# Kernel optimization log

Hardware: AMD Instinct MI355X
Metric: run time of the kernel (lower is better)

Reference implementation:

```python
import jax, jax.numpy as jnp
import numpy as np

B, N, D = 8, 2048, 256

def setup_inputs() -> dict:
    key = jax.random.key(0)
    ks = jax.random.split(key, 8)
    sc = 1.0 / np.sqrt(D)
    return {
        "x": jax.random.normal(ks[0], (B, N, D), dtype=jnp.float32),
        "W_fp": jax.random.normal(ks[1], (D, D), dtype=jnp.float32) * sc,
        "b_fp": jnp.zeros((D,), dtype=jnp.float32),
        "w_s": jax.random.normal(ks[2], (D,), dtype=jnp.float32) * sc,
        "b_s": jnp.zeros((), dtype=jnp.float32),
        "W_rp": jax.random.normal(ks[3], (D, D), dtype=jnp.float32) * sc,
        "b_rp": jnp.zeros((D,), dtype=jnp.float32),
        "W_gp": jax.random.normal(ks[4], (D, D), dtype=jnp.float32) * sc,
        "b_gp": jnp.zeros((D,), dtype=jnp.float32),
        "gamma": jnp.ones((D,), dtype=jnp.float32),
        "beta": jnp.zeros((D,), dtype=jnp.float32),
    }

def reference(x, W_fp, b_fp, w_s, b_s, W_rp, b_rp, W_gp, b_gp, gamma, beta):
    # feature projection: [B, N, D]
    proj = jnp.einsum('bnd,de->bne', x, W_fp) + b_fp
    # F.normalize(p=2, dim=-1) with eps=1e-12
    nrm = jnp.sqrt(jnp.sum(proj * proj, axis=-1, keepdims=True))
    xn = proj / jnp.maximum(nrm, 1e-12)
    # cosine similarity matrix [B, N, N]
    sim = jnp.einsum('bnd,bmd->bnm', xn, xn)
    # adj_scaler: Linear(D,1)+sigmoid is constant along the broadcast axis ->
    # compute per-node scalar once [B, N] (same math as the O(N^2*D) expand)
    s = jax.nn.sigmoid(jnp.einsum('bnd,d->bn', proj, w_s) + b_s)
    scaler = jnp.clip(0.5 * (s[:, :, None] + s[:, None, :]), 1e-6, 1.0)
    adj = jnp.maximum(scaler * sim, 1e-6)  # clamp(min=1e-6)
    degree = jnp.maximum(jnp.sum(adj, axis=2, keepdims=True), 1e-6)
    norm_adj = adj / degree
    # aggregation + region projection
    region = jnp.einsum('bnm,bmd->bnd', norm_adj, proj)
    region = jnp.einsum('bnd,de->bne', region, W_rp) + b_rp
    # global pooling + projection: [B, 1, D]
    g = jnp.mean(region, axis=1, keepdims=True)
    g = jnp.einsum('bnd,de->bne', g, W_gp) + b_gp
    input_global = jnp.mean(x, axis=1, keepdims=True)
    h = g + input_global
    # LayerNorm (eps=1e-5)
    mu = jnp.mean(h, axis=-1, keepdims=True)
    var = jnp.mean((h - mu) ** 2, axis=-1, keepdims=True)
    out = (h - mu) / jnp.sqrt(var + 1e-5) * gamma + beta
    return out, adj
```

## Files before the change

kernel.cpp:

```cpp
#include <hip/hip_runtime.h>
#include <hip/hip_bf16.h>
#include <math.h>

#define Bn 8
#define Nn 2048
#define Dn 256

typedef short short8 __attribute__((ext_vector_type(8)));
typedef float floatx4 __attribute__((ext_vector_type(4)));

__device__ __forceinline__ short f2bf_bits(float f) {
    __bf16 h = (__bf16)f;
    return __builtin_bit_cast(short, h);
}

__device__ __forceinline__ float bf2f(short s) {
    unsigned u = ((unsigned)(unsigned short)s) << 16;
    return __builtin_bit_cast(float, u);
}

__device__ __forceinline__ void gl_lds16(const void* gsrc, void* ldst) {
    __builtin_amdgcn_global_load_lds(
        (const __attribute__((address_space(1))) void*)gsrc,
        (__attribute__((address_space(3))) void*)ldst, 16, 0, 0);
}

__device__ __forceinline__ float sigmoidf_(float z) {
    return 1.0f / (1.0f + __expf(-z));
}


__global__ __launch_bounds__(256) void k_transpose(const float* __restrict__ W,
                                                   short* __restrict__ Wt) {
    __shared__ float Ts[64][65];
    const int t = threadIdx.x;
    const int dt0 = blockIdx.x * 64, et0 = blockIdx.y * 64;
    const int ro = t >> 4, co = (t & 15) * 4;
    #pragma unroll
    for (int rr = 0; rr < 4; ++rr) {
        int row = rr * 16 + ro;
        float4 v = *(const float4*)(W + (size_t)(dt0 + row) * Dn + et0 + co);
        Ts[row][co + 0] = v.x; Ts[row][co + 1] = v.y;
        Ts[row][co + 2] = v.z; Ts[row][co + 3] = v.w;
    }
    __syncthreads();
    const int e = t >> 2, cd0 = (t & 3) * 16;
    short8 a, b;
    #pragma unroll
    for (int i = 0; i < 8; ++i) {
        a[i] = f2bf_bits(Ts[cd0 + i][e]);
        b[i] = f2bf_bits(Ts[cd0 + 8 + i][e]);
    }
    *(short8*)(Wt + (size_t)(et0 + e) * Dn + dt0 + cd0) = a;
    *(short8*)(Wt + (size_t)(et0 + e) * Dn + dt0 + cd0 + 8) = b;
}


__global__ __launch_bounds__(512) void k_projxn(
    const float* __restrict__ x, const short* __restrict__ Wt,
    const float* __restrict__ b_fp, const float* __restrict__ w_s,
    short* __restrict__ xn, float* __restrict__ sdot, float* __restrict__ nrm,
    float* __restrict__ xpart) {
    __shared__ __align__(16) short As[64 * 64];
    __shared__ __align__(16) short Bs[256 * 64];
    __shared__ float xsumS[8 * 256];
    __shared__ float redW[2][64];
    __shared__ float redN[2][64];
    const int t = threadIdx.x;
    const int bm = blockIdx.x * 64;
    const int lane = t & 63, wv = t >> 6;
    const int wm = (wv & 3) * 16;
    const int jh = wv >> 2;
    const int l15 = lane & 15, q = lane >> 4;

    for (int i = t; i < 2048; i += 512) xsumS[i] = 0.f;

    floatx4 acc[8];
    #pragma unroll
    for (int j = 0; j < 8; ++j) acc[j] = (floatx4){0.f, 0.f, 0.f, 0.f};

    const int rA = t >> 3, cA = (t & 7) * 8;
    const int rB = t >> 3, cB = (t & 7) * 8;

    for (int k0 = 0; k0 < Dn; k0 += 64) {
        const float* gp = x + (size_t)(bm + rA) * Dn + k0 + cA;
        float4 v0 = *(const float4*)gp;
        float4 v1 = *(const float4*)(gp + 4);
        short8 o0;
        o0[0] = f2bf_bits(v0.x); o0[1] = f2bf_bits(v0.y);
        o0[2] = f2bf_bits(v0.z); o0[3] = f2bf_bits(v0.w);
        o0[4] = f2bf_bits(v1.x); o0[5] = f2bf_bits(v1.y);
        o0[6] = f2bf_bits(v1.z); o0[7] = f2bf_bits(v1.w);
        *(short8*)(As + rA * 64 + cA) = o0;
        #pragma unroll
        for (int cc = 0; cc < 4; ++cc)
            gl_lds16(Wt + (size_t)(cc * 64 + rB) * Dn + k0 + cB,
                     Bs + (cc * 64 + rB) * 64 + cB);
        __syncthreads();
        #pragma unroll
        for (int ks = 0; ks < 2; ++ks) {
            short8 af = *(const short8*)(As + (wm + l15) * 64 + ks * 32 + q * 8);
            #pragma unroll
            for (int jj = 0; jj < 8; ++jj) {
                short8 bfr = *(const short8*)(Bs + (jh * 128 + jj * 16 + l15) * 64 + ks * 32 + q * 8);
                acc[jj] = __builtin_amdgcn_mfma_f32_16x16x32_bf16(af, bfr, acc[jj], 0, 0, 0);
            }
        }
        {
            float s = 0.f;
            #pragma unroll
            for (int r = 0; r < 8; ++r)
                s += bf2f(As[(wv * 8 + r) * 64 + lane]);
            xsumS[wv * 256 + k0 + lane] += s;
        }
        __syncthreads();
    }
    if (t < 256) {
        float xs = 0.f;
        #pragma unroll
        for (int w = 0; w < 8; ++w) xs += xsumS[w * 256 + t];
        xpart[(size_t)blockIdx.x * Dn + t] = xs;
    }
    float bfv[8], wsv[8];
    #pragma unroll
    for (int jj = 0; jj < 8; ++jj) {
        bfv[jj] = b_fp[jh * 128 + jj * 16 + l15];
        wsv[jj] = w_s[jh * 128 + jj * 16 + l15];
    }
    float vv[4][8];
    #pragma unroll
    for (int reg = 0; reg < 4; ++reg) {
        float pw = 0.f, pn = 0.f;
        #pragma unroll
        for (int jj = 0; jj < 8; ++jj) {
            float v = acc[jj][reg] + bfv[jj];
            vv[reg][jj] = v;
            pw += v * wsv[jj];
            pn += v * v;
        }
        #pragma unroll
        for (int m = 1; m < 16; m <<= 1) {
            pw += __shfl_xor(pw, m);
            pn += __shfl_xor(pn, m);
        }
        if (l15 == 0) {
            redW[jh][wm + q * 4 + reg] = pw;
            redN[jh][wm + q * 4 + reg] = pn;
        }
    }
    __syncthreads();
    #pragma unroll
    for (int reg = 0; reg < 4; ++reg) {
        int lr = wm + q * 4 + reg;
        float pw = redW[0][lr] + redW[1][lr];
        float pn = redN[0][lr] + redN[1][lr];
        float nc = fmaxf(sqrtf(pn), 1e-12f);
        float inv = 1.0f / nc;
        int row = bm + lr;
        size_t rbase = (size_t)row * Dn + jh * 128 + l15;
        #pragma unroll
        for (int jj = 0; jj < 8; ++jj)
            xn[rbase + jj * 16] = f2bf_bits(vv[reg][jj] * inv);
        if (jh == 0 && l15 == 0) {
            sdot[row] = pw;
            nrm[row] = nc;
        }
    }
}


__global__ __launch_bounds__(512) void k_sim(
    const short* __restrict__ xn, const float* __restrict__ sdot,
    const float* __restrict__ b_s, float* __restrict__ adj,
    float* __restrict__ deg_part) {
    __shared__ __align__(16) short As[128 * 64];
    __shared__ __align__(16) short Bs[256 * 64];
    __shared__ float degS[4][128];
    const int t = threadIdx.x;
    int lin = (blockIdx.z * 16 + blockIdx.y) * 8 + blockIdx.x;
    const int b = lin & 7;
    const int pos = lin >> 3;
    const int by = pos >> 3, cx = pos & 7;
    const int bm = by * 128;
    const int bn = cx * 256;
    const int lane = t & 63, wv = t >> 6;
    const int wm = (wv >> 2) * 64;
    const int wn = (wv & 3) * 64;
    const int l15 = lane & 15, q4 = lane >> 4;
    const int rr = t >> 3, c8 = (t & 7) * 8;
    const short* xb = xn + (size_t)b * Nn * Dn;

    floatx4 acc[4][4];
    #pragma unroll
    for (int i = 0; i < 4; ++i)
        #pragma unroll
        for (int j = 0; j < 4; ++j) acc[i][j] = (floatx4){0.f, 0.f, 0.f, 0.f};

    for (int k0 = 0; k0 < Dn; k0 += 64) {
        #pragma unroll
        for (int cc = 0; cc < 2; ++cc) {
            int r = cc * 64 + rr;
            gl_lds16(xb + (size_t)(bm + r) * Dn + k0 + c8, As + r * 64 + c8);
        }
        #pragma unroll
        for (int cc = 0; cc < 4; ++cc) {
            int r = cc * 64 + rr;
            gl_lds16(xb + (size_t)(bn + r) * Dn + k0 + c8, Bs + r * 64 + c8);
        }
        __syncthreads();
        #pragma unroll
        for (int ks = 0; ks < 2; ++ks) {
            short8 af[4], bfr[4];
            #pragma unroll
            for (int i = 0; i < 4; ++i)
                af[i] = *(const short8*)(As + (wm + i * 16 + l15) * 64 + ks * 32 + q4 * 8);
            #pragma unroll
            for (int j = 0; j < 4; ++j)
                bfr[j] = *(const short8*)(Bs + (wn + j * 16 + l15) * 64 + ks * 32 + q4 * 8);
            #pragma unroll
            for (int i = 0; i < 4; ++i)
                #pragma unroll
                for (int j = 0; j < 4; ++j)
                    acc[i][j] = __builtin_amdgcn_mfma_f32_16x16x32_bf16(bfr[j], af[i], acc[i][j], 0, 0, 0);
        }
        __syncthreads();
    }
    const float bsv = b_s[0];
    float srow[4];
    #pragma unroll
    for (int i = 0; i < 4; ++i)
        srow[i] = sigmoidf_(sdot[b * Nn + bm + wm + i * 16 + l15] + bsv);
    float scol[4][4];
    #pragma unroll
    for (int j = 0; j < 4; ++j)
        #pragma unroll
        for (int reg = 0; reg < 4; ++reg)
            scol[j][reg] = sigmoidf_(sdot[b * Nn + bn + wn + j * 16 + q4 * 4 + reg] + bsv);
    #pragma unroll
    for (int i = 0; i < 4; ++i) {
        float rs = 0.f;
        size_t rbase = ((size_t)b * Nn + (bm + wm + i * 16 + l15)) * Nn + bn + wn + q4 * 4;
        #pragma unroll
        for (int j = 0; j < 4; ++j) {
            float4 o;
            float sc;
            sc = fminf(fmaxf(0.5f * (srow[i] + scol[j][0]), 1e-6f), 1.0f);
            o.x = fmaxf(sc * acc[i][j][0], 1e-6f);
            sc = fminf(fmaxf(0.5f * (srow[i] + scol[j][1]), 1e-6f), 1.0f);
            o.y = fmaxf(sc * acc[i][j][1], 1e-6f);
            sc = fminf(fmaxf(0.5f * (srow[i] + scol[j][2]), 1e-6f), 1.0f);
            o.z = fmaxf(sc * acc[i][j][2], 1e-6f);
            sc = fminf(fmaxf(0.5f * (srow[i] + scol[j][3]), 1e-6f), 1.0f);
            o.w = fmaxf(sc * acc[i][j][3], 1e-6f);
            *(float4*)(adj + rbase + (size_t)j * 16) = o;
            rs += o.x + o.y + o.z + o.w;
        }
        rs += __shfl_xor(rs, 16);
        rs += __shfl_xor(rs, 32);
        if (q4 == 0) degS[wv & 3][wm + i * 16 + l15] = rs;
    }
    __syncthreads();
    if (t < 128)
        deg_part[((size_t)(b * 8 + cx)) * Nn + bm + t] =
            degS[0][t] + degS[1][t] + degS[2][t] + degS[3][t];
}


__global__ __launch_bounds__(256) void k_deg(const float* __restrict__ deg_part,
                                             float* __restrict__ invdeg) {
    int b = blockIdx.x, t = blockIdx.y * 256 + threadIdx.x;
    float s = 0.f;
    #pragma unroll
    for (int cx = 0; cx < 8; ++cx)
        s += deg_part[((size_t)(b * 8 + cx)) * Nn + t];
    invdeg[b * Nn + t] = 1.0f / fmaxf(s, 1e-6f);
}


__global__ __launch_bounds__(1024) void k_colsum(
    const float* __restrict__ adj, const float* __restrict__ invdeg,
    const short* __restrict__ xn, const float* __restrict__ nrm,
    float* __restrict__ gpart) {
    int b = blockIdx.x, ck = blockIdx.y, t = threadIdx.x;
    __shared__ float invS[Nn];
    __shared__ float part[64][64];
    __shared__ float csL[64];
    __shared__ float gQ[4][Dn];
    invS[t] = invdeg[b * Nn + t];
    invS[t + 1024] = invdeg[b * Nn + t + 1024];
    __syncthreads();
    const int lc = (t & 15) * 4;
    const int rg = t >> 4;
    const int c0 = ck * 64;
    float sx = 0.f, sy = 0.f, sz = 0.f, sw = 0.f;
    for (int r = rg; r < Nn; r += 64) {
        float4 v = *(const float4*)(adj + ((size_t)b * Nn + r) * Nn + c0 + lc);
        float w = invS[r];
        sx += v.x * w; sy += v.y * w; sz += v.z * w; sw += v.w * w;
    }
    part[rg][lc + 0] = sx; part[rg][lc + 1] = sy;
    part[rg][lc + 2] = sz; part[rg][lc + 3] = sw;
    __syncthreads();
    if (t < 64) {
        float s = 0.f;
        #pragma unroll
        for (int g = 0; g < 64; ++g) s += part[g][t];
        csL[t] = s * nrm[b * Nn + c0 + t];
    }
    __syncthreads();
    {
        int h = t >> 8, d = t & 255;
        float g = 0.f;
        #pragma unroll 4
        for (int mi = 0; mi < 16; ++mi) {
            int m = h * 16 + mi;
            g += csL[m] * bf2f(xn[((size_t)(b * Nn + c0 + m)) * Dn + d]);
        }
        gQ[h][d] = g;
    }
    __syncthreads();
    if (t < Dn)
        gpart[(b * 32 + ck) * Dn + t] = gQ[0][t] + gQ[1][t] + gQ[2][t] + gQ[3][t];
}


__global__ __launch_bounds__(1024) void k_final2(
    const float* __restrict__ gpart, const float* __restrict__ xpart,
    const float* __restrict__ W_rp, const float* __restrict__ b_rp,
    const float* __restrict__ W_gp, const float* __restrict__ b_gp,
    const float* __restrict__ gamma, const float* __restrict__ beta,
    float* __restrict__ out) {
    int b = blockIdx.x, t = threadIdx.x;
    const int d = t & 255, c4 = t >> 8;
    __shared__ float pS[4][Dn];
    __shared__ float xS[4][Dn];
    __shared__ float gp_s[Dn];
    __shared__ float xm_s[Dn];
    __shared__ float g1_s[Dn];
    __shared__ float red[8];
    {
        float gs = 0.f, xs = 0.f;
        #pragma unroll
        for (int k = 0; k < 8; ++k) {
            int ck = c4 * 8 + k;
            gs += gpart[(b * 32 + ck) * Dn + d];
            xs += xpart[(b * 32 + ck) * Dn + d];
        }
        pS[c4][d] = gs;
        xS[c4][d] = xs;
    }
    __syncthreads();
    if (t < Dn) {
        gp_s[t] = (pS[0][t] + pS[1][t] + pS[2][t] + pS[3][t]) * (1.0f / Nn);
        xm_s[t] = (xS[0][t] + xS[1][t] + xS[2][t] + xS[3][t]) * (1.0f / Nn);
    }
    __syncthreads();
    {
        float m1 = 0.f;
        #pragma unroll 4
        for (int i = 0; i < 64; ++i) {
            int dd = c4 * 64 + i;
            m1 += gp_s[dd] * W_rp[dd * Dn + d];
        }
        pS[c4][d] = m1;
    }
    __syncthreads();
    if (t < Dn) g1_s[t] = b_rp[t] + pS[0][t] + pS[1][t] + pS[2][t] + pS[3][t];
    __syncthreads();
    {
        float m2 = 0.f;
        #pragma unroll 4
        for (int i = 0; i < 64; ++i) {
            int ee = c4 * 64 + i;
            m2 += g1_s[ee] * W_gp[ee * Dn + d];
        }
        pS[c4][d] = m2;
    }
    __syncthreads();
    float h = 0.f;
    if (t < Dn) {
        h = b_gp[t] + pS[0][t] + pS[1][t] + pS[2][t] + pS[3][t] + xm_s[t];
        float sum = h;
        #pragma unroll
        for (int m = 1; m < 64; m <<= 1) sum += __shfl_xor(sum, m);
        if ((t & 63) == 0) red[t >> 6] = sum;
    }
    __syncthreads();
    float mu = (red[0] + red[1] + red[2] + red[3]) * (1.0f / Dn);
    if (t < Dn) {
        float dv = h - mu;
        float s2 = dv * dv;
        #pragma unroll
        for (int m = 1; m < 64; m <<= 1) s2 += __shfl_xor(s2, m);
        if ((t & 63) == 0) red[4 + (t >> 6)] = s2;
    }
    __syncthreads();
    if (t < Dn) {
        float dv = h - mu;
        float var = (red[4] + red[5] + red[6] + red[7]) * (1.0f / Dn);
        out[b * Dn + t] = dv * rsqrtf(var + 1e-5f) * gamma[t] + beta[t];
    }
}


extern "C" void kernel_launch(void* const* d_in, const int* in_sizes, int n_in,
                              void* d_out, int out_size, void* d_ws, size_t ws_size,
                              hipStream_t stream) {
    const float* x     = (const float*)d_in[0];
    const float* W_fp  = (const float*)d_in[1];
    const float* b_fp  = (const float*)d_in[2];
    const float* w_s   = (const float*)d_in[3];
    const float* b_s   = (const float*)d_in[4];
    const float* W_rp  = (const float*)d_in[5];
    const float* b_rp  = (const float*)d_in[6];
    const float* W_gp  = (const float*)d_in[7];
    const float* b_gp  = (const float*)d_in[8];
    const float* gamma = (const float*)d_in[9];
    const float* beta  = (const float*)d_in[10];

    float* out = (float*)d_out;
    float* adj = out + Bn * Dn;

    char* ws = (char*)d_ws;
    short* xn     = (short*)(ws);
    short* Wt     = (short*)(ws + 8388608);
    float* sdot   = (float*)(ws + 8519680);
    float* nrm    = (float*)(ws + 8585216);
    float* degp   = (float*)(ws + 8650752);
    float* invdeg = (float*)(ws + 9175040);
    float* gpart  = (float*)(ws + 9699328);
    float* xpart  = (float*)(ws + 9961472);

    k_transpose<<<dim3(4, 4), 256, 0, stream>>>(W_fp, Wt);
    k_projxn<<<(Bn * Nn) / 64, 512, 0, stream>>>(x, Wt, b_fp, w_s, xn, sdot, nrm, xpart);
    k_sim<<<dim3(8, 16, 8), 512, 0, stream>>>(xn, sdot, b_s, adj, degp);
    k_deg<<<dim3(Bn, 8), 256, 0, stream>>>(degp, invdeg);
    k_colsum<<<dim3(Bn, 32), 1024, 0, stream>>>(adj, invdeg, xn, nrm, gpart);
    k_final2<<<Bn, 1024, 0, stream>>>(gpart, xpart, W_rp, b_rp, W_gp, b_gp, gamma, beta, out);
}
```

Before: 237.8 us.

## Fuse all stages into one cooperative persistent kernel with grid syncs

Replaces the six separate kernel launches (transpose, projection, similarity, degree, column-sum, final) with a single cooperative kernel of 256 blocks that runs each stage in turn, separated by grid-wide barriers, and reuses one shared-memory buffer across stages. The goal is to remove launch overhead and inter-kernel gaps. In exchange, parallelism is capped at 256 blocks, so the sim stage loops over tiles and the colsum stage uses 512 threads instead of 1024. The later stages also leave many blocks idle while a few do the work.

```diff
diff --git a/kernel.cpp b/kernel.cpp
--- a/kernel.cpp
+++ b/kernel.cpp
@@ -1,6 +1,9 @@
 #include <hip/hip_runtime.h>
+#include <hip/hip_cooperative_groups.h>
 #include <hip/hip_bf16.h>
 #include <math.h>
+
+namespace cg = cooperative_groups;
 
 #define Bn 8
 #define Nn 2048
@@ -30,375 +33,384 @@
 }
 
 
-__global__ __launch_bounds__(256) void k_transpose(const float* __restrict__ W,
-                                                   short* __restrict__ Wt) {
-    __shared__ float Ts[64][65];
-    const int t = threadIdx.x;
-    const int dt0 = blockIdx.x * 64, et0 = blockIdx.y * 64;
-    const int ro = t >> 4, co = (t & 15) * 4;
-    #pragma unroll
-    for (int rr = 0; rr < 4; ++rr) {
-        int row = rr * 16 + ro;
-        float4 v = *(const float4*)(W + (size_t)(dt0 + row) * Dn + et0 + co);
-        Ts[row][co + 0] = v.x; Ts[row][co + 1] = v.y;
-        Ts[row][co + 2] = v.z; Ts[row][co + 3] = v.w;
-    }
-    __syncthreads();
-    const int e = t >> 2, cd0 = (t & 3) * 16;
-    short8 a, b;
-    #pragma unroll
-    for (int i = 0; i < 8; ++i) {
-        a[i] = f2bf_bits(Ts[cd0 + i][e]);
-        b[i] = f2bf_bits(Ts[cd0 + 8 + i][e]);
-    }
-    *(short8*)(Wt + (size_t)(et0 + e) * Dn + dt0 + cd0) = a;
-    *(short8*)(Wt + (size_t)(et0 + e) * Dn + dt0 + cd0 + 8) = b;
-}
-
-
-__global__ __launch_bounds__(512) void k_projxn(
-    const float* __restrict__ x, const short* __restrict__ Wt,
+__global__ __launch_bounds__(512) void k_fused(
+    const float* __restrict__ x, const float* __restrict__ W_fp,
+    short* __restrict__ Wt,
     const float* __restrict__ b_fp, const float* __restrict__ w_s,
+    const float* __restrict__ b_s,
     short* __restrict__ xn, float* __restrict__ sdot, float* __restrict__ nrm,
-    float* __restrict__ xpart) {
-    __shared__ __align__(16) short As[64 * 64];
-    __shared__ __align__(16) short Bs[256 * 64];
-    __shared__ float xsumS[8 * 256];
-    __shared__ float redW[2][64];
-    __shared__ float redN[2][64];
-    const int t = threadIdx.x;
-    const int bm = blockIdx.x * 64;
-    const int lane = t & 63, wv = t >> 6;
-    const int wm = (wv & 3) * 16;
-    const int jh = wv >> 2;
-    const int l15 = lane & 15, q = lane >> 4;
-
-    for (int i = t; i < 2048; i += 512) xsumS[i] = 0.f;
-
-    floatx4 acc[8];
-    #pragma unroll
-    for (int j = 0; j < 8; ++j) acc[j] = (floatx4){0.f, 0.f, 0.f, 0.f};
-
-    const int rA = t >> 3, cA = (t & 7) * 8;
-    const int rB = t >> 3, cB = (t & 7) * 8;
-
-    for (int k0 = 0; k0 < Dn; k0 += 64) {
-        const float* gp = x + (size_t)(bm + rA) * Dn + k0 + cA;
-        float4 v0 = *(const float4*)gp;
-        float4 v1 = *(const float4*)(gp + 4);
-        short8 o0;
-        o0[0] = f2bf_bits(v0.x); o0[1] = f2bf_bits(v0.y);
-        o0[2] = f2bf_bits(v0.z); o0[3] = f2bf_bits(v0.w);
-        o0[4] = f2bf_bits(v1.x); o0[5] = f2bf_bits(v1.y);
-        o0[6] = f2bf_bits(v1.z); o0[7] = f2bf_bits(v1.w);
-        *(short8*)(As + rA * 64 + cA) = o0;
-        #pragma unroll
-        for (int cc = 0; cc < 4; ++cc)
-            gl_lds16(Wt + (size_t)(cc * 64 + rB) * Dn + k0 + cB,
-                     Bs + (cc * 64 + rB) * 64 + cB);
-        __syncthreads();
-        #pragma unroll
-        for (int ks = 0; ks < 2; ++ks) {
-            short8 af = *(const short8*)(As + (wm + l15) * 64 + ks * 32 + q * 8);
-            #pragma unroll
-            for (int jj = 0; jj < 8; ++jj) {
-                short8 bfr = *(const short8*)(Bs + (jh * 128 + jj * 16 + l15) * 64 + ks * 32 + q * 8);
-                acc[jj] = __builtin_amdgcn_mfma_f32_16x16x32_bf16(af, bfr, acc[jj], 0, 0, 0);
-            }
-        }
-        {
-            float s = 0.f;
-            #pragma unroll
-            for (int r = 0; r < 8; ++r)
-                s += bf2f(As[(wv * 8 + r) * 64 + lane]);
-            xsumS[wv * 256 + k0 + lane] += s;
-        }
-        __syncthreads();
-    }
-    if (t < 256) {
-        float xs = 0.f;
-        #pragma unroll
-        for (int w = 0; w < 8; ++w) xs += xsumS[w * 256 + t];
-        xpart[(size_t)blockIdx.x * Dn + t] = xs;
-    }
-    float bfv[8], wsv[8];
-    #pragma unroll
-    for (int jj = 0; jj < 8; ++jj) {
-        bfv[jj] = b_fp[jh * 128 + jj * 16 + l15];
-        wsv[jj] = w_s[jh * 128 + jj * 16 + l15];
-    }
-    float vv[4][8];
-    #pragma unroll
-    for (int reg = 0; reg < 4; ++reg) {
-        float pw = 0.f, pn = 0.f;
-        #pragma unroll
-        for (int jj = 0; jj < 8; ++jj) {
-            float v = acc[jj][reg] + bfv[jj];
-            vv[reg][jj] = v;
-            pw += v * wsv[jj];
-            pn += v * v;
-        }
-        #pragma unroll
-        for (int m = 1; m < 16; m <<= 1) {
-            pw += __shfl_xor(pw, m);
-            pn += __shfl_xor(pn, m);
-        }
-        if (l15 == 0) {
-            redW[jh][wm + q * 4 + reg] = pw;
-            redN[jh][wm + q * 4 + reg] = pn;
-        }
-    }
-    __syncthreads();
-    #pragma unroll
-    for (int reg = 0; reg < 4; ++reg) {
-        int lr = wm + q * 4 + reg;
-        float pw = redW[0][lr] + redW[1][lr];
-        float pn = redN[0][lr] + redN[1][lr];
-        float nc = fmaxf(sqrtf(pn), 1e-12f);
-        float inv = 1.0f / nc;
-        int row = bm + lr;
-        size_t rbase = (size_t)row * Dn + jh * 128 + l15;
-        #pragma unroll
-        for (int jj = 0; jj < 8; ++jj)
-            xn[rbase + jj * 16] = f2bf_bits(vv[reg][jj] * inv);
-        if (jh == 0 && l15 == 0) {
-            sdot[row] = pw;
-            nrm[row] = nc;
-        }
-    }
-}
-
-
-__global__ __launch_bounds__(512) void k_sim(
-    const short* __restrict__ xn, const float* __restrict__ sdot,
-    const float* __restrict__ b_s, float* __restrict__ adj,
-    float* __restrict__ deg_part) {
-    __shared__ __align__(16) short As[128 * 64];
-    __shared__ __align__(16) short Bs[256 * 64];
-    __shared__ float degS[4][128];
-    const int t = threadIdx.x;
-    int lin = (blockIdx.z * 16 + blockIdx.y) * 8 + blockIdx.x;
-    const int b = lin & 7;
-    const int pos = lin >> 3;
-    const int by = pos >> 3, cx = pos & 7;
-    const int bm = by * 128;
-    const int bn = cx * 256;
-    const int lane = t & 63, wv = t >> 6;
-    const int wm = (wv >> 2) * 64;
-    const int wn = (wv & 3) * 64;
-    const int l15 = lane & 15, q4 = lane >> 4;
-    const int rr = t >> 3, c8 = (t & 7) * 8;
-    const short* xb = xn + (size_t)b * Nn * Dn;
-
-    floatx4 acc[4][4];
-    #pragma unroll
-    for (int i = 0; i < 4; ++i)
-        #pragma unroll
-        for (int j = 0; j < 4; ++j) acc[i][j] = (floatx4){0.f, 0.f, 0.f, 0.f};
-
-    for (int k0 = 0; k0 < Dn; k0 += 64) {
-        #pragma unroll
-        for (int cc = 0; cc < 2; ++cc) {
-            int r = cc * 64 + rr;
-            gl_lds16(xb + (size_t)(bm + r) * Dn + k0 + c8, As + r * 64 + c8);
-        }
-        #pragma unroll
-        for (int cc = 0; cc < 4; ++cc) {
-            int r = cc * 64 + rr;
-            gl_lds16(xb + (size_t)(bn + r) * Dn + k0 + c8, Bs + r * 64 + c8);
-        }
-        __syncthreads();
-        #pragma unroll
-        for (int ks = 0; ks < 2; ++ks) {
-            short8 af[4], bfr[4];
-            #pragma unroll
-            for (int i = 0; i < 4; ++i)
-                af[i] = *(const short8*)(As + (wm + i * 16 + l15) * 64 + ks * 32 + q4 * 8);
-            #pragma unroll
-            for (int j = 0; j < 4; ++j)
-                bfr[j] = *(const short8*)(Bs + (wn + j * 16 + l15) * 64 + ks * 32 + q4 * 8);
-            #pragma unroll
-            for (int i = 0; i < 4; ++i)
-                #pragma unroll
-                for (int j = 0; j < 4; ++j)
-                    acc[i][j] = __builtin_amdgcn_mfma_f32_16x16x32_bf16(bfr[j], af[i], acc[i][j], 0, 0, 0);
-        }
-        __syncthreads();
-    }
-    const float bsv = b_s[0];
-    float srow[4];
-    #pragma unroll
-    for (int i = 0; i < 4; ++i)
-        srow[i] = sigmoidf_(sdot[b * Nn + bm + wm + i * 16 + l15] + bsv);
-    float scol[4][4];
-    #pragma unroll
-    for (int j = 0; j < 4; ++j)
-        #pragma unroll
-        for (int reg = 0; reg < 4; ++reg)
-            scol[j][reg] = sigmoidf_(sdot[b * Nn + bn + wn + j * 16 + q4 * 4 + reg] + bsv);
-    #pragma unroll
-    for (int i = 0; i < 4; ++i) {
-        float rs = 0.f;
-        size_t rbase = ((size_t)b * Nn + (bm + wm + i * 16 + l15)) * Nn + bn + wn + q4 * 4;
-        #pragma unroll
-        for (int j = 0; j < 4; ++j) {
-            float4 o;
-            float sc;
-            sc = fminf(fmaxf(0.5f * (srow[i] + scol[j][0]), 1e-6f), 1.0f);
-            o.x = fmaxf(sc * acc[i][j][0], 1e-6f);
-            sc = fminf(fmaxf(0.5f * (srow[i] + scol[j][1]), 1e-6f), 1.0f);
-            o.y = fmaxf(sc * acc[i][j][1], 1e-6f);
-            sc = fminf(fmaxf(0.5f * (srow[i] + scol[j][2]), 1e-6f), 1.0f);
-            o.z = fmaxf(sc * acc[i][j][2], 1e-6f);
-            sc = fminf(fmaxf(0.5f * (srow[i] + scol[j][3]), 1e-6f), 1.0f);
-            o.w = fmaxf(sc * acc[i][j][3], 1e-6f);
-            *(float4*)(adj + rbase + (size_t)j * 16) = o;
-            rs += o.x + o.y + o.z + o.w;
-        }
-        rs += __shfl_xor(rs, 16);
-        rs += __shfl_xor(rs, 32);
-        if (q4 == 0) degS[wv & 3][wm + i * 16 + l15] = rs;
-    }
-    __syncthreads();
-    if (t < 128)
-        deg_part[((size_t)(b * 8 + cx)) * Nn + bm + t] =
-            degS[0][t] + degS[1][t] + degS[2][t] + degS[3][t];
-}
-
-
-__global__ __launch_bounds__(256) void k_deg(const float* __restrict__ deg_part,
-                                             float* __restrict__ invdeg) {
-    int b = blockIdx.x, t = blockIdx.y * 256 + threadIdx.x;
-    float s = 0.f;
-    #pragma unroll
-    for (int cx = 0; cx < 8; ++cx)
-        s += deg_part[((size_t)(b * 8 + cx)) * Nn + t];
-    invdeg[b * Nn + t] = 1.0f / fmaxf(s, 1e-6f);
-}
-
-
-__global__ __launch_bounds__(1024) void k_colsum(
-    const float* __restrict__ adj, const float* __restrict__ invdeg,
-    const short* __restrict__ xn, const float* __restrict__ nrm,
-    float* __restrict__ gpart) {
-    int b = blockIdx.x, ck = blockIdx.y, t = threadIdx.x;
-    __shared__ float invS[Nn];
-    __shared__ float part[64][64];
-    __shared__ float csL[64];
-    __shared__ float gQ[4][Dn];
-    invS[t] = invdeg[b * Nn + t];
-    invS[t + 1024] = invdeg[b * Nn + t + 1024];
-    __syncthreads();
-    const int lc = (t & 15) * 4;
-    const int rg = t >> 4;
-    const int c0 = ck * 64;
-    float sx = 0.f, sy = 0.f, sz = 0.f, sw = 0.f;
-    for (int r = rg; r < Nn; r += 64) {
-        float4 v = *(const float4*)(adj + ((size_t)b * Nn + r) * Nn + c0 + lc);
-        float w = invS[r];
-        sx += v.x * w; sy += v.y * w; sz += v.z * w; sw += v.w * w;
-    }
-    part[rg][lc + 0] = sx; part[rg][lc + 1] = sy;
-    part[rg][lc + 2] = sz; part[rg][lc + 3] = sw;
-    __syncthreads();
-    if (t < 64) {
-        float s = 0.f;
-        #pragma unroll
-        for (int g = 0; g < 64; ++g) s += part[g][t];
-        csL[t] = s * nrm[b * Nn + c0 + t];
-    }
-    __syncthreads();
-    {
-        int h = t >> 8, d = t & 255;
-        float g = 0.f;
-        #pragma unroll 4
-        for (int mi = 0; mi < 16; ++mi) {
-            int m = h * 16 + mi;
-            g += csL[m] * bf2f(xn[((size_t)(b * Nn + c0 + m)) * Dn + d]);
-        }
-        gQ[h][d] = g;
-    }
-    __syncthreads();
-    if (t < Dn)
-        gpart[(b * 32 + ck) * Dn + t] = gQ[0][t] + gQ[1][t] + gQ[2][t] + gQ[3][t];
-}
-
-
-__global__ __launch_bounds__(1024) void k_final2(
-    const float* __restrict__ gpart, const float* __restrict__ xpart,
+    float* __restrict__ xpart,
+    float* __restrict__ adj, float* __restrict__ degp,
+    float* __restrict__ invdeg, float* __restrict__ gpart,
     const float* __restrict__ W_rp, const float* __restrict__ b_rp,
     const float* __restrict__ W_gp, const float* __restrict__ b_gp,
     const float* __restrict__ gamma, const float* __restrict__ beta,
     float* __restrict__ out) {
-    int b = blockIdx.x, t = threadIdx.x;
-    const int d = t & 255, c4 = t >> 8;
-    __shared__ float pS[4][Dn];
-    __shared__ float xS[4][Dn];
-    __shared__ float gp_s[Dn];
-    __shared__ float xm_s[Dn];
-    __shared__ float g1_s[Dn];
-    __shared__ float red[8];
+    cg::grid_group grid = cg::this_grid();
+    __shared__ __align__(16) char SM[51200];
+    const int t = threadIdx.x;
+    const int bid = blockIdx.x;
+    const int lane = t & 63, wv = t >> 6;
+    const int l15 = lane & 15, q = lane >> 4;
+
+    if (bid < 16) {
+        float (*Ts)[65] = (float(*)[65])SM;
+        const int dt0 = (bid >> 2) * 64, et0 = (bid & 3) * 64;
+        if (t < 256) {
+            const int ro = t >> 4, co = (t & 15) * 4;
+            #pragma unroll
+            for (int rr = 0; rr < 4; ++rr) {
+                int row = rr * 16 + ro;
+                float4 v = *(const float4*)(W_fp + (size_t)(dt0 + row) * Dn + et0 + co);
+                Ts[row][co + 0] = v.x; Ts[row][co + 1] = v.y;
+                Ts[row][co + 2] = v.z; Ts[row][co + 3] = v.w;
+            }
+        }
+        __syncthreads();
+        if (t < 256) {
+            const int e = t >> 2, cd0 = (t & 3) * 16;
+            short8 a, b;
+            #pragma unroll
+            for (int i = 0; i < 8; ++i) {
+                a[i] = f2bf_bits(Ts[cd0 + i][e]);
+                b[i] = f2bf_bits(Ts[cd0 + 8 + i][e]);
+            }
+            *(short8*)(Wt + (size_t)(et0 + e) * Dn + dt0 + cd0) = a;
+            *(short8*)(Wt + (size_t)(et0 + e) * Dn + dt0 + cd0 + 8) = b;
+        }
+    }
+    grid.sync();
+
     {
-        float gs = 0.f, xs = 0.f;
-        #pragma unroll
-        for (int k = 0; k < 8; ++k) {
-            int ck = c4 * 8 + k;
-            gs += gpart[(b * 32 + ck) * Dn + d];
-            xs += xpart[(b * 32 + ck) * Dn + d];
-        }
-        pS[c4][d] = gs;
-        xS[c4][d] = xs;
-    }
-    __syncthreads();
-    if (t < Dn) {
-        gp_s[t] = (pS[0][t] + pS[1][t] + pS[2][t] + pS[3][t]) * (1.0f / Nn);
-        xm_s[t] = (xS[0][t] + xS[1][t] + xS[2][t] + xS[3][t]) * (1.0f / Nn);
-    }
-    __syncthreads();
+        short* As = (short*)SM;
+        short* Bs = (short*)(SM + 8192);
+        float* xsumS = (float*)(SM + 40960);
+        float* redW = (float*)(SM + 49152);
+        float* redN = (float*)(SM + 49664);
+        const int bm = bid * 64;
+        const int wm = (wv & 3) * 16;
+        const int jh = wv >> 2;
+
+        for (int i = t; i < 2048; i += 512) xsumS[i] = 0.f;
+
+        floatx4 acc[8];
+        #pragma unroll
+        for (int j = 0; j < 8; ++j) acc[j] = (floatx4){0.f, 0.f, 0.f, 0.f};
+
+        const int rA = t >> 3, cA = (t & 7) * 8;
+        const int rB = t >> 3, cB = (t & 7) * 8;
+
+        for (int k0 = 0; k0 < Dn; k0 += 64) {
+            const float* gp = x + (size_t)(bm + rA) * Dn + k0 + cA;
+            float4 v0 = *(const float4*)gp;
+            float4 v1 = *(const float4*)(gp + 4);
+            short8 o0;
+            o0[0] = f2bf_bits(v0.x); o0[1] = f2bf_bits(v0.y);
+            o0[2] = f2bf_bits(v0.z); o0[3] = f2bf_bits(v0.w);
+            o0[4] = f2bf_bits(v1.x); o0[5] = f2bf_bits(v1.y);
+            o0[6] = f2bf_bits(v1.z); o0[7] = f2bf_bits(v1.w);
+            *(short8*)(As + rA * 64 + cA) = o0;
+            #pragma unroll
+            for (int cc = 0; cc < 4; ++cc)
+                gl_lds16(Wt + (size_t)(cc * 64 + rB) * Dn + k0 + cB,
+                         Bs + (cc * 64 + rB) * 64 + cB);
+            __syncthreads();
+            #pragma unroll
+            for (int ks = 0; ks < 2; ++ks) {
+                short8 af = *(const short8*)(As + (wm + l15) * 64 + ks * 32 + q * 8);
+                #pragma unroll
+                for (int jj = 0; jj < 8; ++jj) {
+                    short8 bfr = *(const short8*)(Bs + (jh * 128 + jj * 16 + l15) * 64 + ks * 32 + q * 8);
+                    acc[jj] = __builtin_amdgcn_mfma_f32_16x16x32_bf16(af, bfr, acc[jj], 0, 0, 0);
+                }
+            }
+            {
+                float s = 0.f;
+                #pragma unroll
+                for (int r = 0; r < 8; ++r)
+                    s += bf2f(As[(wv * 8 + r) * 64 + lane]);
+                xsumS[wv * 256 + k0 + lane] += s;
+            }
+            __syncthreads();
+        }
+        if (t < 256) {
+            float xs = 0.f;
+            #pragma unroll
+            for (int w = 0; w < 8; ++w) xs += xsumS[w * 256 + t];
+            xpart[(size_t)bid * Dn + t] = xs;
+        }
+        float bfv[8], wsv[8];
+        #pragma unroll
+        for (int jj = 0; jj < 8; ++jj) {
+            bfv[jj] = b_fp[jh * 128 + jj * 16 + l15];
+            wsv[jj] = w_s[jh * 128 + jj * 16 + l15];
+        }
+        float vv[4][8];
+        #pragma unroll
+        for (int reg = 0; reg < 4; ++reg) {
+            float pw = 0.f, pn = 0.f;
+            #pragma unroll
+            for (int jj = 0; jj < 8; ++jj) {
+                float v = acc[jj][reg] + bfv[jj];
+                vv[reg][jj] = v;
+                pw += v * wsv[jj];
+                pn += v * v;
+            }
+            #pragma unroll
+            for (int m = 1; m < 16; m <<= 1) {
+                pw += __shfl_xor(pw, m);
+                pn += __shfl_xor(pn, m);
+            }
+            if (l15 == 0) {
+                redW[jh * 64 + wm + q * 4 + reg] = pw;
+                redN[jh * 64 + wm + q * 4 + reg] = pn;
+            }
+        }
+        __syncthreads();
+        #pragma unroll
+        for (int reg = 0; reg < 4; ++reg) {
+            int lr = wm + q * 4 + reg;
+            float pw = redW[lr] + redW[64 + lr];
+            float pn = redN[lr] + redN[64 + lr];
+            float nc = fmaxf(sqrtf(pn), 1e-12f);
+            float inv = 1.0f / nc;
+            int row = bm + lr;
+            size_t rbase = (size_t)row * Dn + jh * 128 + l15;
+            #pragma unroll
+            for (int jj = 0; jj < 8; ++jj)
+                xn[rbase + jj * 16] = f2bf_bits(vv[reg][jj] * inv);
+            if (jh == 0 && l15 == 0) {
+                sdot[row] = pw;
+                nrm[row] = nc;
+            }
+        }
+    }
+    grid.sync();
+
     {
-        float m1 = 0.f;
-        #pragma unroll 4
-        for (int i = 0; i < 64; ++i) {
-            int dd = c4 * 64 + i;
-            m1 += gp_s[dd] * W_rp[dd * Dn + d];
-        }
-        pS[c4][d] = m1;
-    }
-    __syncthreads();
-    if (t < Dn) g1_s[t] = b_rp[t] + pS[0][t] + pS[1][t] + pS[2][t] + pS[3][t];
-    __syncthreads();
+        short* As = (short*)SM;
+        short* Bs = (short*)(SM + 16384);
+        float* degS = (float*)(SM + 49152);
+        const int b = bid & 7;
+        const int wm = (wv >> 2) * 64;
+        const int wn = (wv & 3) * 64;
+        const int q4 = lane >> 4;
+        const int rr = t >> 3, c8 = (t & 7) * 8;
+        const short* xb = xn + (size_t)b * Nn * Dn;
+        const float bsv = b_s[0];
+
+        for (int vi = 0; vi < 4; ++vi) {
+            const int pos = (bid >> 3) * 4 + vi;
+            const int by = pos >> 3, cx = pos & 7;
+            const int bm = by * 128;
+            const int bn = cx * 256;
+
+            floatx4 acc[4][4];
+            #pragma unroll
+            for (int i = 0; i < 4; ++i)
+                #pragma unroll
+                for (int j = 0; j < 4; ++j) acc[i][j] = (floatx4){0.f, 0.f, 0.f, 0.f};
+
+            for (int k0 = 0; k0 < Dn; k0 += 64) {
+                #pragma unroll
+                for (int cc = 0; cc < 2; ++cc) {
+                    int r = cc * 64 + rr;
+                    gl_lds16(xb + (size_t)(bm + r) * Dn + k0 + c8, As + r * 64 + c8);
+                }
+                #pragma unroll
+                for (int cc = 0; cc < 4; ++cc) {
+                    int r = cc * 64 + rr;
+                    gl_lds16(xb + (size_t)(bn + r) * Dn + k0 + c8, Bs + r * 64 + c8);
+                }
+                __syncthreads();
+                #pragma unroll
+                for (int ks = 0; ks < 2; ++ks) {
+                    short8 af[4], bfr[4];
+                    #pragma unroll
+                    for (int i = 0; i < 4; ++i)
+                        af[i] = *(const short8*)(As + (wm + i * 16 + l15) * 64 + ks * 32 + q4 * 8);
+                    #pragma unroll
+                    for (int j = 0; j < 4; ++j)
+                        bfr[j] = *(const short8*)(Bs + (wn + j * 16 + l15) * 64 + ks * 32 + q4 * 8);
+                    #pragma unroll
+                    for (int i = 0; i < 4; ++i)
+                        #pragma unroll
+                        for (int j = 0; j < 4; ++j)
+                            acc[i][j] = __builtin_amdgcn_mfma_f32_16x16x32_bf16(bfr[j], af[i], acc[i][j], 0, 0, 0);
+                }
+                __syncthreads();
+            }
+            float srow[4];
+            #pragma unroll
+            for (int i = 0; i < 4; ++i)
+                srow[i] = sigmoidf_(sdot[b * Nn + bm + wm + i * 16 + l15] + bsv);
+            float scol[4][4];
+            #pragma unroll
+            for (int j = 0; j < 4; ++j)
+                #pragma unroll
+                for (int reg = 0; reg < 4; ++reg)
+                    scol[j][reg] = sigmoidf_(sdot[b * Nn + bn + wn + j * 16 + q4 * 4 + reg] + bsv);
+            #pragma unroll
+            for (int i = 0; i < 4; ++i) {
+                float rs = 0.f;
+                size_t rbase = ((size_t)b * Nn + (bm + wm + i * 16 + l15)) * Nn + bn + wn + q4 * 4;
+                #pragma unroll
+                for (int j = 0; j < 4; ++j) {
+                    float4 o;
+                    float sc;
+                    sc = fminf(fmaxf(0.5f * (srow[i] + scol[j][0]), 1e-6f), 1.0f);
+                    o.x = fmaxf(sc * acc[i][j][0], 1e-6f);
+                    sc = fminf(fmaxf(0.5f * (srow[i] + scol[j][1]), 1e-6f), 1.0f);
+                    o.y = fmaxf(sc * acc[i][j][1], 1e-6f);
+                    sc = fminf(fmaxf(0.5f * (srow[i] + scol[j][2]), 1e-6f), 1.0f);
+                    o.z = fmaxf(sc * acc[i][j][2], 1e-6f);
+                    sc = fminf(fmaxf(0.5f * (srow[i] + scol[j][3]), 1e-6f), 1.0f);
+                    o.w = fmaxf(sc * acc[i][j][3], 1e-6f);
+                    *(float4*)(adj + rbase + (size_t)j * 16) = o;
+                    rs += o.x + o.y + o.z + o.w;
+                }
+                rs += __shfl_xor(rs, 16);
+                rs += __shfl_xor(rs, 32);
+                if (q4 == 0) degS[(wv & 3) * 128 + wm + i * 16 + l15] = rs;
+            }
+            __syncthreads();
+            if (t < 128)
+                degp[((size_t)(b * 8 + cx)) * Nn + bm + t] =
+                    degS[t] + degS[128 + t] + degS[256 + t] + degS[384 + t];
+            __syncthreads();
+        }
+    }
+    grid.sync();
+
+    if (bid < 32) {
+        int idx = bid * 512 + t;
+        int b = idx >> 11, r = idx & 2047;
+        float s = 0.f;
+        #pragma unroll
+        for (int cx = 0; cx < 8; ++cx)
+            s += degp[((size_t)(b * 8 + cx)) * Nn + r];
+        invdeg[b * Nn + r] = 1.0f / fmaxf(s, 1e-6f);
+    }
+    grid.sync();
+
     {
-        float m2 = 0.f;
-        #pragma unroll 4
-        for (int i = 0; i < 64; ++i) {
-            int ee = c4 * 64 + i;
-            m2 += g1_s[ee] * W_gp[ee * Dn + d];
-        }
-        pS[c4][d] = m2;
-    }
-    __syncthreads();
-    float h = 0.f;
-    if (t < Dn) {
-        h = b_gp[t] + pS[0][t] + pS[1][t] + pS[2][t] + pS[3][t] + xm_s[t];
-        float sum = h;
-        #pragma unroll
-        for (int m = 1; m < 64; m <<= 1) sum += __shfl_xor(sum, m);
-        if ((t & 63) == 0) red[t >> 6] = sum;
-    }
-    __syncthreads();
-    float mu = (red[0] + red[1] + red[2] + red[3]) * (1.0f / Dn);
-    if (t < Dn) {
-        float dv = h - mu;
-        float s2 = dv * dv;
-        #pragma unroll
-        for (int m = 1; m < 64; m <<= 1) s2 += __shfl_xor(s2, m);
-        if ((t & 63) == 0) red[4 + (t >> 6)] = s2;
-    }
-    __syncthreads();
-    if (t < Dn) {
-        float dv = h - mu;
-        float var = (red[4] + red[5] + red[6] + red[7]) * (1.0f / Dn);
-        out[b * Dn + t] = dv * rsqrtf(var + 1e-5f) * gamma[t] + beta[t];
+        float* invS = (float*)SM;
+        float (*part)[64] = (float(*)[64])(SM + 8192);
+        float* csL = (float*)(SM + 16384);
+        float* gHalf = (float*)(SM + 16640);
+        const int b = bid & 7, ck = bid >> 3;
+        #pragma unroll
+        for (int rc = 0; rc < 4; ++rc) {
+            int row = rc * 512 + t;
+            invS[row] = invdeg[b * Nn + row];
+        }
+        __syncthreads();
+        const int lc = (t & 15) * 4;
+        const int rg = t >> 4;
+        const int c0 = ck * 64;
+        float sx = 0.f, sy = 0.f, sz = 0.f, sw = 0.f;
+        for (int r = rg; r < Nn; r += 32) {
+            float4 v = *(const float4*)(adj + ((size_t)b * Nn + r) * Nn + c0 + lc);
+            float w = invS[r];
+            sx += v.x * w; sy += v.y * w; sz += v.z * w; sw += v.w * w;
+        }
+        part[rg][lc + 0] = sx; part[rg][lc + 1] = sy;
+        part[rg][lc + 2] = sz; part[rg][lc + 3] = sw;
+        __syncthreads();
+        if (t < 64) {
+            float s = 0.f;
+            #pragma unroll
+            for (int g = 0; g < 32; ++g) s += part[g][t];
+            csL[t] = s * nrm[b * Nn + c0 + t];
+        }
+        __syncthreads();
+        {
+            int h = t >> 8, d = t & 255;
+            float g = 0.f;
+            #pragma unroll 4
+            for (int mi = 0; mi < 32; ++mi) {
+                int m = h * 32 + mi;
+                g += csL[m] * bf2f(xn[((size_t)(b * Nn + c0 + m)) * Dn + d]);
+            }
+            gHalf[h * 256 + d] = g;
+        }
+        __syncthreads();
+        if (t < Dn)
+            gpart[(b * 32 + ck) * Dn + t] = gHalf[t] + gHalf[256 + t];
+    }
+    grid.sync();
+
+    if (bid < Bn) {
+        const int b = bid;
+        float* pS = (float*)SM;
+        float* xS = (float*)(SM + 2048);
+        float* gp_s = (float*)(SM + 4096);
+        float* xm_s = (float*)(SM + 5120);
+        float* g1_s = (float*)(SM + 6144);
+        float* red = (float*)(SM + 7168);
+        const int d = t & 255, c2 = t >> 8;
+        {
+            float gs = 0.f, xs = 0.f;
+            #pragma unroll
+            for (int k = 0; k < 16; ++k) {
+                int ck = c2 * 16 + k;
+                gs += gpart[(b * 32 + ck) * Dn + d];
+                xs += xpart[(b * 32 + ck) * Dn + d];
+            }
+            pS[c2 * 256 + d] = gs;
+            xS[c2 * 256 + d] = xs;
+        }
+        __syncthreads();
+        if (t < Dn) {
+            gp_s[t] = (pS[t] + pS[256 + t]) * (1.0f / Nn);
+            xm_s[t] = (xS[t] + xS[256 + t]) * (1.0f / Nn);
+        }
+        __syncthreads();
+        {
+            float m1 = 0.f;
+            #pragma unroll 4
+            for (int i = 0; i < 128; ++i) {
+                int dd = c2 * 128 + i;
+                m1 += gp_s[dd] * W_rp[dd * Dn + d];
+            }
+            pS[c2 * 256 + d] = m1;
+        }
+        __syncthreads();
+        if (t < Dn) g1_s[t] = b_rp[t] + pS[t] + pS[256 + t];
+        __syncthreads();
+        {
+            float m2 = 0.f;
+            #pragma unroll 4
+            for (int i = 0; i < 128; ++i) {
+                int ee = c2 * 128 + i;
+                m2 += g1_s[ee] * W_gp[ee * Dn + d];
+            }
+            pS[c2 * 256 + d] = m2;
+        }
+        __syncthreads();
+        float h = 0.f;
+        if (t < Dn) {
+            h = b_gp[t] + pS[t] + pS[256 + t] + xm_s[t];
+            float sum = h;
+            #pragma unroll
+            for (int m = 1; m < 64; m <<= 1) sum += __shfl_xor(sum, m);
+            if ((t & 63) == 0) red[t >> 6] = sum;
+        }
+        __syncthreads();
+        float mu = (red[0] + red[1] + red[2] + red[3]) * (1.0f / Dn);
+        if (t < Dn) {
+            float dv = h - mu;
+            float s2 = dv * dv;
+            #pragma unroll
+            for (int m = 1; m < 64; m <<= 1) s2 += __shfl_xor(s2, m);
+            if ((t & 63) == 0) red[4 + (t >> 6)] = s2;
+        }
+        __syncthreads();
+        if (t < Dn) {
+            float dv = h - mu;
+            float var = (red[4] + red[5] + red[6] + red[7]) * (1.0f / Dn);
+            out[b * Dn + t] = dv * rsqrtf(var + 1e-5f) * gamma[t] + beta[t];
+        }
     }
 }
 
@@ -431,10 +443,12 @@
     float* gpart  = (float*)(ws + 9699328);
     float* xpart  = (float*)(ws + 9961472);
 
-    k_transpose<<<dim3(4, 4), 256, 0, stream>>>(W_fp, Wt);
-    k_projxn<<<(Bn * Nn) / 64, 512, 0, stream>>>(x, Wt, b_fp, w_s, xn, sdot, nrm, xpart);
-    k_sim<<<dim3(8, 16, 8), 512, 0, stream>>>(xn, sdot, b_s, adj, degp);
-    k_deg<<<dim3(Bn, 8), 256, 0, stream>>>(degp, invdeg);
-    k_colsum<<<dim3(Bn, 32), 1024, 0, stream>>>(adj, invdeg, xn, nrm, gpart);
-    k_final2<<<Bn, 1024, 0, stream>>>(gpart, xpart, W_rp, b_rp, W_gp, b_gp, gamma, beta, out);
-}
+    void* args[] = {
+        (void*)&x, (void*)&W_fp, (void*)&Wt, (void*)&b_fp, (void*)&w_s,
+        (void*)&b_s, (void*)&xn, (void*)&sdot, (void*)&nrm, (void*)&xpart,
+        (void*)&adj, (void*)&degp, (void*)&invdeg, (void*)&gpart,
+        (void*)&W_rp, (void*)&b_rp, (void*)&W_gp, (void*)&b_gp,
+        (void*)&gamma, (void*)&beta, (void*)&out
+    };
+    hipLaunchCooperativeKernel(k_fused, dim3(256), dim3(512), args, 0, stream);
+}
```

After: 430.6 us. 81.1% more time.
